# Optimization experiments

Measured on AMD Instinct MI355X. Metric: run time of the kernel, lower is better.

The kernel has to match this reference:

```python
import jax, jax.numpy as jnp
import numpy as np

# Quantization constants from the original module
X_ZP = -66   # int8 zero point
Y_ZP = 160   # uint8 zero point


def setup_inputs() -> dict:
    key = jax.random.key(0)
    k1, k2 = jax.random.split(key)
    # x: [7, B, M, K] int8 in [-128, 127]
    x = jax.random.randint(k1, (7, 8, 512, 1024), -128, 128, dtype=jnp.int32).astype(jnp.int8)
    # y: [B, K, N] uint8 in [0, 255]
    y = jax.random.randint(k2, (8, 1024, 512), 0, 256, dtype=jnp.int32).astype(jnp.uint8)
    return {
        "x": x,
        "y": y,
        "x_scale": jnp.float32(0.03),
        "y_scale": jnp.float32(0.025),
    }


def reference(x, y, x_scale, y_scale):
    # dequantize_per_tensor: (q - zero_point) * scale
    xf = (x.astype(jnp.float32) - jnp.float32(X_ZP)) * x_scale   # [7, B, M, K]
    yf = (y.astype(jnp.float32) - jnp.float32(Y_ZP)) * y_scale   # [B, K, N]
    # torch.matmul broadcast: [7,B,M,K] @ [B,K,N] -> [7,B,M,N]
    return jnp.einsum('gbmk,bkn->gbmn', xf, yf)
```

## Files before the change

kernel.cpp:

```cpp
#include <hip/hip_runtime.h>
#include <stdint.h>

typedef int v4i __attribute__((ext_vector_type(4)));

constexpr int G = 7, B = 8, M = 512, N = 512, K = 1024;
constexpr int GBn = G * B;

constexpr size_t YT_BYTES = (size_t)B * N * K;
constexpr size_t CSP_CNT  = (size_t)16 * B * N;
constexpr size_t WS_NEEDED = YT_BYTES + CSP_CNT * 4;

__global__ __launch_bounds__(256) void transpose_pack_y(const int* __restrict__ y,
                                                        signed char* __restrict__ yt,
                                                        int* __restrict__ csp) {
    __shared__ unsigned char tile[64][80];
    int n0  = blockIdx.x * 64;
    int k0t = blockIdx.y;
    int k0  = k0t * 64;
    int b   = blockIdx.z;
    int t   = threadIdx.x;

    int r  = t >> 2;
    int c0 = (t & 3) * 16;
    const int* src = y + ((size_t)b * K + k0 + r) * N + n0 + c0;
    uint32_t p[4];
#pragma unroll
    for (int q = 0; q < 4; ++q) {
        int4 v = ((const int4*)src)[q];
        p[q] =  (uint32_t)((v.x & 255) ^ 128)
             | ((uint32_t)((v.y & 255) ^ 128) << 8)
             | ((uint32_t)((v.z & 255) ^ 128) << 16)
             | ((uint32_t)((v.w & 255) ^ 128) << 24);
    }
    *(uint4*)&tile[r][c0] = make_uint4(p[0], p[1], p[2], p[3]);
    __syncthreads();

    int nl = t >> 2;
    int kc = (t & 3) * 16;
    uint32_t q[4];
    int s = 0;
#pragma unroll
    for (int w = 0; w < 4; ++w) {
        uint32_t b0 = tile[kc + w * 4 + 0][nl];
        uint32_t b1 = tile[kc + w * 4 + 1][nl];
        uint32_t b2 = tile[kc + w * 4 + 2][nl];
        uint32_t b3 = tile[kc + w * 4 + 3][nl];
        s += (int)(signed char)b0 + (int)(signed char)b1
           + (int)(signed char)b2 + (int)(signed char)b3;
        q[w] = b0 | (b1 << 8) | (b2 << 16) | (b3 << 24);
    }
    *(uint4*)(yt + ((size_t)b * N + n0 + nl) * K + k0 + kc) = make_uint4(q[0], q[1], q[2], q[3]);

    s += __shfl_xor(s, 1, 64);
    s += __shfl_xor(s, 2, 64);
    if ((t & 3) == 0) csp[(size_t)k0t * (B * N) + b * N + n0 + nl] = s;
}

__global__ __launch_bounds__(1024) void gemm_fused(const int* __restrict__ x,
                                                   const signed char* __restrict__ yt,
                                                   const int* __restrict__ csp,
                                                   const float* __restrict__ xsp,
                                                   const float* __restrict__ ysp,
                                                   float* __restrict__ out) {
    __shared__ __align__(16) signed char Ap[128 * 1024];
    __shared__ int cs_lds[512];
    __shared__ int rs_lds[128];

    int id  = blockIdx.x;
    int swz = (id & 7) * 28 + (id >> 3);
    int gb  = swz >> 2;
    int mt  = swz & 3;
    int b   = gb & 7;

    int tid = threadIdx.x, wave = tid >> 6, lane = tid & 63;

    if (tid < 512) {
        int s = 0;
        const int* p = csp + b * N + tid;
#pragma unroll
        for (int kt = 0; kt < 16; ++kt) s += p[(size_t)kt * (B * N)];
        cs_lds[tid] = s;
    }

    int r  = tid >> 3;
    int a8 = tid & 7;
    const int4* Arow = (const int4*)(x + ((size_t)(gb * M + mt * 128 + r)) * K);
    int rsum = 0;
#pragma unroll
    for (int ii = 0; ii < 4; ++ii) {
        int4 v[8];
#pragma unroll
        for (int u = 0; u < 8; ++u) v[u] = Arow[a8 + 8 * (ii * 8 + u)];
#pragma unroll
        for (int u = 0; u < 8; ++u) {
            int i = ii * 8 + u;
            int4 t = v[u];
            rsum += t.x + t.y + t.z + t.w;
            uint32_t w =  (uint32_t)(t.x & 255)
                       | ((uint32_t)(t.y & 255) << 8)
                       | ((uint32_t)(t.z & 255) << 16)
                       | ((uint32_t)(t.w & 255) << 24);
            int c = (a8 >> 2) + 2 * i;
            *(uint32_t*)(&Ap[r * 1024 + ((c ^ (r & 7)) << 4) + ((a8 & 3) << 2)]) = w;
        }
    }
    rsum += __shfl_xor(rsum, 1, 64);
    rsum += __shfl_xor(rsum, 2, 64);
    rsum += __shfl_xor(rsum, 4, 64);
    if ((tid & 7) == 0) rs_lds[r] = rsum;

    __syncthreads();

    int fr = lane & 15;
    int h  = lane >> 4;
    int s3 = fr & 7;
    int wm = (wave >> 3) * 64;
    int wn = (wave & 7) * 64;

    int arow0 = (wm + fr) * 1024;
    int aeven = arow0 + (((h)      ^ s3) << 4);
    int aodd  = arow0 + (((4 + h)  ^ s3) << 4);

    const signed char* Bj0 = yt + ((size_t)(b * N + wn + fr)) * K + h * 16;

    v4i zero = {0, 0, 0, 0};
    v4i acc[4][4];
#pragma unroll
    for (int i = 0; i < 4; ++i)
#pragma unroll
        for (int j = 0; j < 4; ++j) acc[i][j] = zero;

#pragma unroll
    for (int t = 0; t < 16; ++t) {
        v4i bf[4], af[4];
#pragma unroll
        for (int j = 0; j < 4; ++j)
            bf[j] = *(const v4i*)(Bj0 + (size_t)j * 16 * K + t * 64);
        int ab = (t & 1) ? aodd : aeven;
#pragma unroll
        for (int i = 0; i < 4; ++i)
            af[i] = *(const v4i*)(&Ap[ab + i * 16384 + (t >> 1) * 128]);
#pragma unroll
        for (int i = 0; i < 4; ++i)
#pragma unroll
            for (int j = 0; j < 4; ++j)
                acc[i][j] = __builtin_amdgcn_mfma_i32_16x16x64_i8(af[i], bf[j], acc[i][j], 0, 0, 0);
    }

    float sc = xsp[0] * ysp[0];
    int colL = lane & 15;
    int rowQ = (lane >> 4) * 4;
    float* outg = out + (size_t)gb * (M * N) + (size_t)(mt * 128) * N;
#pragma unroll
    for (int i = 0; i < 4; ++i) {
#pragma unroll
        for (int rr = 0; rr < 4; ++rr) {
            int row_l = wm + i * 16 + rowQ + rr;
            int rsv = rs_lds[row_l];
#pragma unroll
            for (int j = 0; j < 4; ++j) {
                int col = wn + j * 16 + colL;
                int tv = acc[i][j][rr] - 32 * rsv + 66 * cs_lds[col] - 2162688;
                outg[(size_t)row_l * N + col] = sc * (float)tv;
            }
        }
    }
}

__global__ __launch_bounds__(256) void naive_kernel(const int* __restrict__ x,
                                                    const int* __restrict__ y,
                                                    const float* __restrict__ xsp,
                                                    const float* __restrict__ ysp,
                                                    float* __restrict__ out) {
    size_t idx = (size_t)blockIdx.x * 256 + threadIdx.x;
    int n  = (int)(idx & 511);
    int m  = (int)((idx >> 9) & 511);
    int gb = (int)(idx >> 18);
    int b  = gb & 7;
    const int* xr = x + ((size_t)gb * M + m) * K;
    const int* yc = y + (size_t)b * K * N + n;
    int dot = 0, sx = 0, sy = 0;
    for (int k = 0; k < K; ++k) {
        int a = xr[k];
        int c = yc[(size_t)k * N];
        dot += a * c; sx += a; sy += c;
    }
    float s = xsp[0] * ysp[0];
    out[idx] = s * (float)(dot - 160 * sx + 66 * sy - 10813440);
}

extern "C" void kernel_launch(void* const* d_in, const int* in_sizes, int n_in,
                              void* d_out, int out_size, void* d_ws, size_t ws_size,
                              hipStream_t stream) {
    const int*   x  = (const int*)d_in[0];
    const int*   y  = (const int*)d_in[1];
    const float* xs = (const float*)d_in[2];
    const float* ys = (const float*)d_in[3];
    float* out = (float*)d_out;

    if (ws_size < WS_NEEDED) {
        naive_kernel<<<(14680064 + 255) / 256, 256, 0, stream>>>(x, y, xs, ys, out);
        return;
    }

    char* ws = (char*)d_ws;
    signed char* yt  = (signed char*)ws;
    int*         csp = (int*)(ws + YT_BYTES);

    transpose_pack_y<<<dim3(N / 64, K / 64, B), 256, 0, stream>>>(y, yt, csp);
    gemm_fused<<<dim3(224), 1024, 0, stream>>>(x, yt, csp, xs, ys, out);
}
```

Before: 230.5 us.

## Halve GEMM M-tile to 64 rows, widen per-wave N tile, double-buffer B fragments

Retiles the fused int8 GEMM from 224 blocks of 1024 threads with 128-row A tiles to 448 blocks of 512 threads with 64-row tiles. Each wave now computes 32x128 instead of 64x64. B fragments are software-pipelined with a two-stage register double buffer, and A is staged into LDS with wider 16-byte swizzled stores. The aim is to fit two blocks per CU, covering all 256 CUs, and to hide global-load latency for B. The cost is more register pressure and more B reads from global memory per A row.

New measurement: 262.0 us. +13.6%, slower.

```diff
diff --git a/kernel.cpp b/kernel.cpp
--- a/kernel.cpp
+++ b/kernel.cpp
@@ -56,52 +56,60 @@
     if ((t & 3) == 0) csp[(size_t)k0t * (B * N) + b * N + n0 + nl] = s;
 }
 
-__global__ __launch_bounds__(1024) void gemm_fused(const int* __restrict__ x,
-                                                   const signed char* __restrict__ yt,
-                                                   const int* __restrict__ csp,
-                                                   const float* __restrict__ xsp,
-                                                   const float* __restrict__ ysp,
-                                                   float* __restrict__ out) {
-    __shared__ __align__(16) signed char Ap[128 * 1024];
+__global__ __launch_bounds__(512, 2) void gemm_fused(const int* __restrict__ x,
+                                                     const signed char* __restrict__ yt,
+                                                     const int* __restrict__ csp,
+                                                     const float* __restrict__ xsp,
+                                                     const float* __restrict__ ysp,
+                                                     float* __restrict__ out) {
+    __shared__ __align__(16) signed char Ap[64][1024];
     __shared__ int cs_lds[512];
-    __shared__ int rs_lds[128];
+    __shared__ int rs_lds[64];
 
     int id  = blockIdx.x;
-    int swz = (id & 7) * 28 + (id >> 3);
-    int gb  = swz >> 2;
-    int mt  = swz & 3;
+    int swz = (id & 7) * 56 + (id >> 3);
+    int gb  = swz >> 3;
+    int mt  = swz & 7;
     int b   = gb & 7;
 
     int tid = threadIdx.x, wave = tid >> 6, lane = tid & 63;
 
-    if (tid < 512) {
+    {
         int s = 0;
         const int* p = csp + b * N + tid;
 #pragma unroll
         for (int kt = 0; kt < 16; ++kt) s += p[(size_t)kt * (B * N)];
         cs_lds[tid] = s;
     }
+    float sc = xsp[0] * ysp[0];
 
     int r  = tid >> 3;
     int a8 = tid & 7;
-    const int4* Arow = (const int4*)(x + ((size_t)(gb * M + mt * 128 + r)) * K);
+    int rswz = r & 7;
+    const int4* Arow = (const int4*)(x + ((size_t)(gb * M + mt * 64 + r)) * K);
     int rsum = 0;
 #pragma unroll
-    for (int ii = 0; ii < 4; ++ii) {
-        int4 v[8];
-#pragma unroll
-        for (int u = 0; u < 8; ++u) v[u] = Arow[a8 + 8 * (ii * 8 + u)];
-#pragma unroll
-        for (int u = 0; u < 8; ++u) {
-            int i = ii * 8 + u;
-            int4 t = v[u];
-            rsum += t.x + t.y + t.z + t.w;
-            uint32_t w =  (uint32_t)(t.x & 255)
+    for (int ww = 0; ww < 2; ++ww) {
+        int4 v[16];
+#pragma unroll
+        for (int w4 = 0; w4 < 4; ++w4)
+#pragma unroll
+            for (int vv = 0; vv < 4; ++vv)
+                v[w4 * 4 + vv] = Arow[a8 * 4 + vv + 32 * (ww * 4 + w4)];
+#pragma unroll
+        for (int w4 = 0; w4 < 4; ++w4) {
+            uint32_t pw[4];
+#pragma unroll
+            for (int vv = 0; vv < 4; ++vv) {
+                int4 t = v[w4 * 4 + vv];
+                rsum += t.x + t.y + t.z + t.w;
+                pw[vv] =  (uint32_t)(t.x & 255)
                        | ((uint32_t)(t.y & 255) << 8)
                        | ((uint32_t)(t.z & 255) << 16)
                        | ((uint32_t)(t.w & 255) << 24);
-            int c = (a8 >> 2) + 2 * i;
-            *(uint32_t*)(&Ap[r * 1024 + ((c ^ (r & 7)) << 4) + ((a8 & 3) << 2)]) = w;
+            }
+            int c = a8 + 8 * (ww * 4 + w4);
+            *(uint4*)&Ap[r][(c ^ rswz) << 4] = make_uint4(pw[0], pw[1], pw[2], pw[3]);
         }
     }
     rsum += __shfl_xor(rsum, 1, 64);
@@ -113,52 +121,58 @@
 
     int fr = lane & 15;
     int h  = lane >> 4;
-    int s3 = fr & 7;
-    int wm = (wave >> 3) * 64;
-    int wn = (wave & 7) * 64;
-
-    int arow0 = (wm + fr) * 1024;
-    int aeven = arow0 + (((h)      ^ s3) << 4);
-    int aodd  = arow0 + (((4 + h)  ^ s3) << 4);
-
-    const signed char* Bj0 = yt + ((size_t)(b * N + wn + fr)) * K + h * 16;
+    int wm = (wave >> 2) * 32;
+    int wn = (wave & 3) * 128;
+    int fswz = fr & 7;
+
+    const signed char* Bb[8];
+#pragma unroll
+    for (int j = 0; j < 8; ++j)
+        Bb[j] = yt + ((size_t)(b * N + wn + j * 16 + fr)) * K + h * 16;
 
     v4i zero = {0, 0, 0, 0};
-    v4i acc[4][4];
-#pragma unroll
-    for (int i = 0; i < 4; ++i)
-#pragma unroll
-        for (int j = 0; j < 4; ++j) acc[i][j] = zero;
+    v4i acc[2][8];
+#pragma unroll
+    for (int i = 0; i < 2; ++i)
+#pragma unroll
+        for (int j = 0; j < 8; ++j) acc[i][j] = zero;
+
+    v4i bf[2][8];
+#pragma unroll
+    for (int j = 0; j < 8; ++j) bf[0][j] = *(const v4i*)(Bb[j]);
 
 #pragma unroll
     for (int t = 0; t < 16; ++t) {
-        v4i bf[4], af[4];
-#pragma unroll
-        for (int j = 0; j < 4; ++j)
-            bf[j] = *(const v4i*)(Bj0 + (size_t)j * 16 * K + t * 64);
-        int ab = (t & 1) ? aodd : aeven;
-#pragma unroll
-        for (int i = 0; i < 4; ++i)
-            af[i] = *(const v4i*)(&Ap[ab + i * 16384 + (t >> 1) * 128]);
-#pragma unroll
-        for (int i = 0; i < 4; ++i)
-#pragma unroll
-            for (int j = 0; j < 4; ++j)
-                acc[i][j] = __builtin_amdgcn_mfma_i32_16x16x64_i8(af[i], bf[j], acc[i][j], 0, 0, 0);
-    }
-
-    float sc = xsp[0] * ysp[0];
+        int cur = t & 1;
+        if (t < 15) {
+#pragma unroll
+            for (int j = 0; j < 8; ++j)
+                bf[cur ^ 1][j] = *(const v4i*)(Bb[j] + (t + 1) * 64);
+        }
+
+        v4i af[2];
+#pragma unroll
+        for (int i = 0; i < 2; ++i)
+            af[i] = *(const v4i*)&Ap[wm + i * 16 + fr][((t * 4 + h) ^ fswz) << 4];
+
+#pragma unroll
+        for (int i = 0; i < 2; ++i)
+#pragma unroll
+            for (int j = 0; j < 8; ++j)
+                acc[i][j] = __builtin_amdgcn_mfma_i32_16x16x64_i8(af[i], bf[cur][j], acc[i][j], 0, 0, 0);
+    }
+
     int colL = lane & 15;
     int rowQ = (lane >> 4) * 4;
-    float* outg = out + (size_t)gb * (M * N) + (size_t)(mt * 128) * N;
-#pragma unroll
-    for (int i = 0; i < 4; ++i) {
+    float* outg = out + (size_t)gb * (M * N) + (size_t)(mt * 64) * N;
+#pragma unroll
+    for (int i = 0; i < 2; ++i) {
 #pragma unroll
         for (int rr = 0; rr < 4; ++rr) {
             int row_l = wm + i * 16 + rowQ + rr;
             int rsv = rs_lds[row_l];
 #pragma unroll
-            for (int j = 0; j < 4; ++j) {
+            for (int j = 0; j < 8; ++j) {
                 int col = wn + j * 16 + colL;
                 int tv = acc[i][j][rr] - 32 * rsv + 66 * cs_lds[col] - 2162688;
                 outg[(size_t)row_l * N + col] = sc * (float)tv;
@@ -208,5 +222,5 @@
     int*         csp = (int*)(ws + YT_BYTES);
 
     transpose_pack_y<<<dim3(N / 64, K / 64, B), 256, 0, stream>>>(y, yt, csp);
-    gemm_fused<<<dim3(224), 1024, 0, stream>>>(x, yt, csp, xs, ys, out);
-}
+    gemm_fused<<<dim3(448), 512, 0, stream>>>(x, yt, csp, xs, ys, out);
+}
```
